# Optimization experiments

Measured on AMD Instinct MI355X. Metric: run time of the kernel, lower is better.

The kernel has to match this reference:

```python
import jax, jax.numpy as jnp
import numpy as np

N = 50000   # nodes
E = 800000  # edges
D = 128     # node_channels


def setup_inputs() -> dict:
    key = jax.random.key(0)
    ks = jax.random.split(key, 16)
    s = 1.0 / np.sqrt(D)
    inp = {
        "x": jax.random.normal(ks[0], (N, D), dtype=jnp.float32),
        "edge_index": jax.random.randint(ks[1], (2, E), 0, N, dtype=jnp.int64),
        "eps": jax.random.normal(ks[2], (N, D), dtype=jnp.float32),
    }
    names = ["1", "2", "mu", "logstd", "5", "6"]
    for i, nm in enumerate(names):
        inp[f"W{nm}"] = jax.random.normal(ks[3 + 2 * i], (D, D), dtype=jnp.float32) * s
        inp[f"b{nm}"] = jnp.zeros((D,), dtype=jnp.float32)
    return inp


def _gcn_norm(edge_index, num_nodes):
    # add self-loops, then symmetric normalization deg^{-1/2} (A+I) deg^{-1/2}
    loop = jnp.arange(num_nodes, dtype=edge_index.dtype)
    src = jnp.concatenate([edge_index[0], loop])
    dst = jnp.concatenate([edge_index[1], loop])
    deg = jax.ops.segment_sum(jnp.ones_like(src, dtype=jnp.float32), dst,
                              num_segments=num_nodes)
    dis = jnp.where(deg > 0, jax.lax.rsqrt(deg), 0.0)
    norm = dis[src] * dis[dst]  # [E + N]
    return src, dst, norm


def _gcn(x, W, b, src, dst, norm, num_nodes):
    h = x @ W                              # [N, D] small GEMM
    msg = h[src] * norm[:, None]           # gather + scale, [E+N, D]
    out = jax.ops.segment_sum(msg, dst, num_segments=num_nodes)  # scatter-add
    return out + b


def reference(x, edge_index, eps, W1, b1, W2, b2, Wmu, bmu, Wlogstd, blogstd,
              W5, b5, W6, b6):
    num_nodes = x.shape[0]
    src, dst, norm = _gcn_norm(edge_index, num_nodes)
    g = lambda h, W, b: _gcn(h, W, b, src, dst, norm, num_nodes)

    nodes = jax.nn.relu(g(x, W1, b1))
    nodes = jax.nn.relu(g(nodes, W2, b2))
    mu = g(nodes, Wmu, bmu)
    logstd = g(nodes, Wlogstd, blogstd)
    # reparametrize (training mode), divider = 10
    nodes = mu + eps * jnp.exp(logstd) / 10.0
    nodes = jax.nn.relu(g(nodes, W5, b5))
    nodes = jax.nn.relu(g(nodes, W6, b6))
    return nodes
```

## Files before the change

### kernel.cpp

```cpp
#include <hip/hip_runtime.h>
#include <hip/hip_bf16.h>
#include <cstdint>
#include <cstddef>

#define D 128
#define NWG 200

typedef _Float16 f16;
typedef f16 f16x2 __attribute__((ext_vector_type(2)));
typedef f16 f16x4 __attribute__((ext_vector_type(4)));
typedef f16 f16x8 __attribute__((ext_vector_type(8)));
typedef float f32x4 __attribute__((ext_vector_type(4)));

static inline size_t align256(size_t x){ return (x + 255) & ~(size_t)255; }

__global__ void detect_kernel(const int* __restrict__ ei, long long n32, int* __restrict__ flag){
  __shared__ int s;
  if (threadIdx.x == 0) s = 0;
  __syncthreads();
  int nz = 0;
  for (long long i = 2LL*threadIdx.x + 1; i < 4096 && i < n32; i += 512)
    nz |= (ei[i] != 0);
  if (nz) s = 1;
  __syncthreads();
  if (threadIdx.x == 0) *flag = (s ? 0 : 1);
}

__device__ __forceinline__ void load_edge(const void* ei, int E, int is64, int e, int& s, int& d){
  if (is64) {
    const long long* p = (const long long*)ei;
    s = (int)p[e]; d = (int)p[(size_t)E + e];
  } else {
    const int* p = (const int*)ei;
    s = p[e]; d = p[(size_t)E + e];
  }
}

__global__ __launch_bounds__(256) void passA_hist(
    const void* __restrict__ ei, int E, const int* __restrict__ flag,
    int* __restrict__ glob_hist, int NB){
  __shared__ int cnt[256];
  int t = threadIdx.x, wg = blockIdx.x;
  cnt[t] = 0;
  __syncthreads();
  int is64 = *flag;
  int chunk = (E + NWG - 1) / NWG;
  int lo = wg * chunk, hi = min(lo + chunk, E);
  for (int e = lo + t; e < hi; e += 256){
    int s, d;
    load_edge(ei, E, is64, e, s, d);
    atomicAdd(&cnt[d >> 8], 1);
  }
  __syncthreads();
  for (int b = t; b < NB; b += 256)
    glob_hist[b * NWG + wg] = cnt[b];
}

__global__ void scan_partial(const int* __restrict__ src, int* __restrict__ dst,
                             int* __restrict__ blockSums, int L){
  __shared__ int sd[256];
  int t = threadIdx.x;
  int base = blockIdx.x * 1024 + t * 4;
  int v[4]; int s = 0;
  #pragma unroll
  for (int j = 0; j < 4; ++j){ v[j] = (base + j < L) ? src[base + j] : 0; s += v[j]; }
  sd[t] = s; __syncthreads();
  for (int off = 1; off < 256; off <<= 1){
    int x = (t >= off) ? sd[t - off] : 0;
    __syncthreads();
    sd[t] += x;
    __syncthreads();
  }
  int run = sd[t] - s;
  #pragma unroll
  for (int j = 0; j < 4; ++j){
    if (base + j < L) dst[base + j] = run;
    run += v[j];
  }
  if (t == 255) blockSums[blockIdx.x] = sd[255];
}

__global__ void scan_blocksums(int* __restrict__ blockSums, int nblk,
                               int* __restrict__ dst, int L, int total){
  __shared__ int sd[256];
  int t = threadIdx.x;
  int v = (t < nblk) ? blockSums[t] : 0;
  sd[t] = v; __syncthreads();
  for (int off = 1; off < 256; off <<= 1){
    int x = (t >= off) ? sd[t - off] : 0;
    __syncthreads();
    sd[t] += x;
    __syncthreads();
  }
  if (t < nblk) blockSums[t] = sd[t] - v;
  if (t == 0) dst[L] = total;
}

__global__ void scan_add(int* __restrict__ dst, const int* __restrict__ blockSums, int L){
  int i = blockIdx.x * blockDim.x + threadIdx.x;
  if (i >= L) return;
  dst[i] += blockSums[i >> 10];
}

__global__ __launch_bounds__(256) void passB_scatter(
    const void* __restrict__ ei, int E, const int* __restrict__ flag,
    const int* __restrict__ bucketOff, int NB, unsigned* __restrict__ packed){
  __shared__ int cur[256];
  int t = threadIdx.x, wg = blockIdx.x;
  for (int b = t; b < NB; b += 256)
    cur[b] = bucketOff[b * NWG + wg];
  __syncthreads();
  int is64 = *flag;
  int chunk = (E + NWG - 1) / NWG;
  int lo = wg * chunk, hi = min(lo + chunk, E);
  for (int e = lo + t; e < hi; e += 256){
    int s, d;
    load_edge(ei, E, is64, e, s, d);
    int pos = atomicAdd(&cur[d >> 8], 1);
    packed[pos] = (unsigned)s | ((unsigned)(d & 255) << 16);
  }
}

__global__ __launch_bounds__(256) void passC_csr(
    const unsigned* __restrict__ packed, const int* __restrict__ bucketOff,
    int NB, int N, int E,
    int* __restrict__ rowptr, float* __restrict__ dis, int* __restrict__ csr_src){
  __shared__ int degl[256];
  __shared__ int sd[256];
  __shared__ int cur[256];
  int t = threadIdx.x, b = blockIdx.x;
  int begin = bucketOff[(size_t)b * NWG];
  int endb  = bucketOff[(size_t)(b + 1) * NWG];
  degl[t] = 0;
  __syncthreads();
  for (int i = begin + t; i < endb; i += 256)
    atomicAdd(&degl[(packed[i] >> 16) & 255], 1);
  __syncthreads();
  int dv = degl[t];
  sd[t] = dv; __syncthreads();
  for (int off = 1; off < 256; off <<= 1){
    int x = (t >= off) ? sd[t - off] : 0;
    __syncthreads();
    sd[t] += x;
    __syncthreads();
  }
  int localOff = sd[t] - dv;
  int v = b * 256 + t;
  if (v < N){
    rowptr[v] = begin + localOff;
    dis[v] = rsqrtf((float)(dv + 1));
  }
  if (b == NB - 1 && t == 0) rowptr[N] = E;
  cur[t] = begin + localOff;
  __syncthreads();
  for (int i = begin + t; i < endb; i += 256){
    unsigned p = packed[i];
    int pos = atomicAdd(&cur[(p >> 16) & 255], 1);
    csr_src[pos] = (int)(p & 0xFFFFu);
  }
}

__global__ void cast_scale(const float* __restrict__ in, const float* __restrict__ dis,
                           f16* __restrict__ out, int n4){
  int i = blockIdx.x * blockDim.x + threadIdx.x;
  if (i >= n4) return;
  float dv = dis[i >> 5];
  float4 v = ((const float4*)in)[i];
  f16x4 o; o[0]=(f16)(v.x*dv); o[1]=(f16)(v.y*dv); o[2]=(f16)(v.z*dv); o[3]=(f16)(v.w*dv);
  ((f16x4*)out)[i] = o;
}

__global__ void prep_w(const float* __restrict__ Wa, const float* __restrict__ Wb,
                       const float* __restrict__ Wc, const float* __restrict__ Wd,
                       const float* __restrict__ We, const float* __restrict__ Wf,
                       f16* __restrict__ Wt){
  int i = blockIdx.x * 256 + threadIdx.x;
  int w = i >> 14, rem = i & 16383;
  int n = rem >> 7, k = rem & 127;
  const float* Wp = (w==0)?Wa:(w==1)?Wb:(w==2)?Wc:(w==3)?Wd:(w==4)?We:Wf;
  Wt[i] = (f16)Wp[k*128 + n];
}

__global__ __launch_bounds__(256) void agg16(
    const f16* __restrict__ in, f16* __restrict__ out,
    const int* __restrict__ rowptr, const int* __restrict__ csr_src,
    const float* __restrict__ dis, int N){
  int v = blockIdx.x * 4 + (threadIdx.x >> 6);
  if (v >= N) return;
  int c2 = (threadIdx.x & 63) * 2;
  float dv = dis[v];
  int beg = rowptr[v], end = rowptr[v + 1];
  f16x2 sv = *(const f16x2*)&in[(size_t)v * D + c2];
  float acc0 = (float)sv[0], acc1 = (float)sv[1];
  int e = beg;
  for (; e + 7 < end; e += 8){
    f16x2 h[8];
    #pragma unroll
    for (int j = 0; j < 8; ++j){
      int u = csr_src[e + j];
      h[j] = *(const f16x2*)&in[(size_t)u * D + c2];
    }
    #pragma unroll
    for (int j = 0; j < 8; ++j){ acc0 += (float)h[j][0]; acc1 += (float)h[j][1]; }
  }
  for (; e + 1 < end; e += 2){
    int u0 = csr_src[e], u1 = csr_src[e + 1];
    f16x2 h0 = *(const f16x2*)&in[(size_t)u0 * D + c2];
    f16x2 h1 = *(const f16x2*)&in[(size_t)u1 * D + c2];
    acc0 += (float)h0[0] + (float)h1[0];
    acc1 += (float)h0[1] + (float)h1[1];
  }
  if (e < end){
    int u = csr_src[e];
    f16x2 h = *(const f16x2*)&in[(size_t)u * D + c2];
    acc0 += (float)h[0]; acc1 += (float)h[1];
  }
  f16x2 o; o[0] = (f16)(acc0 * dv); o[1] = (f16)(acc1 * dv);
  *(f16x2*)&out[(size_t)v * D + c2] = o;
}

template<int EPI>
__global__ __launch_bounds__(512) void gemm_mfma(
    const f16* __restrict__ A, const f16* __restrict__ Wt, const float* __restrict__ bias,
    const f16* __restrict__ Wt2, const float* __restrict__ bias2,
    const float* __restrict__ eps, const float* __restrict__ dis,
    f16* __restrict__ out16, float* __restrict__ outf, int N){

  extern __shared__ __align__(16) f16 Ws[];

  int t = threadIdx.x;
  int wave = t >> 6, lane = t & 63;
  int lrow = lane & 15, hi = lane >> 4;
  int r0 = blockIdx.x * 128 + wave * 16;
  bool active = (r0 < N);

  f16x8 a[4];
  if (active){
    int rr = min(r0 + lrow, N - 1);
    const f16* arow = &A[(size_t)rr * D + hi * 8];
    #pragma unroll
    for (int s = 0; s < 4; ++s) a[s] = *(const f16x8*)&arow[s * 32];
  }

  {
    int r = t & 127, p = t >> 7;
    const float4* src = (const float4*)&Wt[r * 128 + p * 32];
    f16* dstrow = &Ws[r * 128];
    #pragma unroll
    for (int i = 0; i < 4; ++i){
      int q = p * 4 + i;
      *(float4*)&dstrow[(q ^ (r & 7)) * 8] = src[i];
    }
    if (EPI == 1){
      const float4* src2 = (const float4*)&Wt2[r * 128 + p * 32];
      f16* dstrow2 = &Ws[16384 + r * 128];
      #pragma unroll
      for (int i = 0; i < 4; ++i){
        int q = p * 4 + i;
        *(float4*)&dstrow2[(q ^ (r & 7)) * 8] = src2[i];
      }
    }
  }
  __syncthreads();
  if (!active) return;

  f32x4 acc[8] = {};
  f32x4 acc2[8] = {};

  #pragma unroll
  for (int s = 0; s < 4; ++s){
    #pragma unroll
    for (int tt = 0; tt < 8; ++tt){
      int n = tt * 16 + lrow;
      int q = (s * 4 + hi) ^ (lrow & 7);
      f16x8 b = *(const f16x8*)&Ws[n * 128 + q * 8];
      acc[tt] = __builtin_amdgcn_mfma_f32_16x16x32_f16(b, a[s], acc[tt], 0, 0, 0);
      if (EPI == 1){
        f16x8 b2 = *(const f16x8*)&Ws[16384 + n * 128 + q * 8];
        acc2[tt] = __builtin_amdgcn_mfma_f32_16x16x32_f16(b2, a[s], acc2[tt], 0, 0, 0);
      }
    }
  }

  int r = r0 + lrow;
  if (r >= N) return;
  float dv = (EPI == 2) ? 1.f : dis[r];
  int cbase = hi * 4;
  #pragma unroll
  for (int tt = 0; tt < 8; ++tt){
    int n0 = tt * 16 + cbase;
    f32x4 bv = *(const f32x4*)&bias[n0];
    if (EPI == 0){
      f16x4 o;
      #pragma unroll
      for (int ii = 0; ii < 4; ++ii)
        o[ii] = (f16)(fmaxf(acc[tt][ii] + bv[ii], 0.f) * dv);
      *(f16x4*)&out16[(size_t)r * D + n0] = o;
    } else if (EPI == 1){
      f32x4 bv2 = *(const f32x4*)&bias2[n0];
      f32x4 e4  = *(const f32x4*)&eps[(size_t)r * D + n0];
      f16x4 o;
      #pragma unroll
      for (int ii = 0; ii < 4; ++ii){
        float mu = acc[tt][ii] + bv[ii];
        float ls = acc2[tt][ii] + bv2[ii];
        o[ii] = (f16)((mu + e4[ii] * __expf(ls) * 0.1f) * dv);
      }
      *(f16x4*)&out16[(size_t)r * D + n0] = o;
    } else {
      f32x4 o;
      #pragma unroll
      for (int ii = 0; ii < 4; ++ii)
        o[ii] = fmaxf(acc[tt][ii] + bv[ii], 0.f);
      *(f32x4*)&outf[(size_t)r * D + n0] = o;
    }
  }
}

extern "C" void kernel_launch(void* const* d_in, const int* in_sizes, int n_in,
                              void* d_out, int out_size, void* d_ws, size_t ws_size,
                              hipStream_t stream){
  const float* x   = (const float*)d_in[0];
  const void*  ei  = d_in[1];
  const float* eps = (const float*)d_in[2];
  const float* W1  = (const float*)d_in[3];  const float* b1  = (const float*)d_in[4];
  const float* W2  = (const float*)d_in[5];  const float* b2  = (const float*)d_in[6];
  const float* Wmu = (const float*)d_in[7];  const float* bmu = (const float*)d_in[8];
  const float* Wls = (const float*)d_in[9];  const float* bls = (const float*)d_in[10];
  const float* W5  = (const float*)d_in[11]; const float* b5  = (const float*)d_in[12];
  const float* W6  = (const float*)d_in[13]; const float* b6  = (const float*)d_in[14];

  const int N = in_sizes[0] / D;
  const int E = in_sizes[1] / 2;
  const int NB = (N + 255) >> 8;
  const int L  = NB * NWG;
  float* out = (float*)d_out;

  char* ws = (char*)d_ws;
  size_t off = 0;
  auto alloc = [&](size_t bytes){ char* p = ws + off; off += align256(bytes); return p; };
  int*      flag      = (int*)     alloc(256);
  int*      glob_hist = (int*)     alloc(((size_t)L + 1) * 4);
  int*      bucketOff = (int*)     alloc(((size_t)L + 1) * 4);
  int*      blockSums = (int*)     alloc(1024);
  int*      rowptr    = (int*)     alloc(((size_t)N + 1) * 4);
  float*    dis       = (float*)   alloc((size_t)N * 4);
  unsigned* packed    = (unsigned*)alloc((size_t)E * 4);
  int*      csr_src   = (int*)     alloc((size_t)E * 4);
  f16*      Wt        = (f16*)     alloc((size_t)6 * 128 * 128 * 2);
  f16*      bufA      = (f16*)     alloc((size_t)N * D * 2);
  f16*      bufB      = (f16*)     alloc((size_t)N * D * 2);
  (void)ws_size; (void)n_in; (void)out_size;

  detect_kernel<<<1, 256, 0, stream>>>((const int*)ei, (long long)2 * E, flag);

  passA_hist<<<NWG, 256, 0, stream>>>(ei, E, flag, glob_hist, NB);
  int nblk = (L + 1023) / 1024;
  scan_partial<<<nblk, 256, 0, stream>>>(glob_hist, bucketOff, blockSums, L);
  scan_blocksums<<<1, 256, 0, stream>>>(blockSums, nblk, bucketOff, L, E);
  scan_add<<<(L + 255) / 256, 256, 0, stream>>>(bucketOff, blockSums, L);
  passB_scatter<<<NWG, 256, 0, stream>>>(ei, E, flag, bucketOff, NB, packed);
  passC_csr<<<NB, 256, 0, stream>>>(packed, bucketOff, NB, N, E, rowptr, dis, csr_src);

  cast_scale<<<(N * D / 4 + 255) / 256, 256, 0, stream>>>(x, dis, bufB, N * D / 4);
  prep_w<<<(6 * 16384) / 256, 256, 0, stream>>>(W1, W2, Wmu, Wls, W5, W6, Wt);

  int aggGrid = (N + 3) / 4;
  int gemmGrid = (N + 127) / 128;
  size_t lds1 = 128 * 128 * sizeof(f16);
  size_t lds2 = 2 * 128 * 128 * sizeof(f16);

  agg16<<<aggGrid, 256, 0, stream>>>(bufB, bufA, rowptr, csr_src, dis, N);
  gemm_mfma<0><<<gemmGrid, 512, lds1, stream>>>(bufA, Wt + 0*16384, b1, nullptr, nullptr, nullptr, dis, bufB, nullptr, N);
  agg16<<<aggGrid, 256, 0, stream>>>(bufB, bufA, rowptr, csr_src, dis, N);
  gemm_mfma<0><<<gemmGrid, 512, lds1, stream>>>(bufA, Wt + 1*16384, b2, nullptr, nullptr, nullptr, dis, bufB, nullptr, N);
  agg16<<<aggGrid, 256, 0, stream>>>(bufB, bufA, rowptr, csr_src, dis, N);
  gemm_mfma<1><<<gemmGrid, 512, lds2, stream>>>(bufA, Wt + 2*16384, bmu, Wt + 3*16384, bls, eps, dis, bufB, nullptr, N);
  agg16<<<aggGrid, 256, 0, stream>>>(bufB, bufA, rowptr, csr_src, dis, N);
  gemm_mfma<0><<<gemmGrid, 512, lds1, stream>>>(bufA, Wt + 4*16384, b5, nullptr, nullptr, nullptr, dis, bufB, nullptr, N);
  agg16<<<aggGrid, 256, 0, stream>>>(bufB, bufA, rowptr, csr_src, dis, N);
  gemm_mfma<2><<<gemmGrid, 512, lds1, stream>>>(bufA, Wt + 5*16384, b6, nullptr, nullptr, nullptr, dis, nullptr, out, N);
}
```

Measured before the change: 396.6 us.

## Drop detect and scan_add launches, use 16-bit CSR indices, widen aggregation unroll

Removes the detect_kernel and scan_add launches. The int64 check becomes a per-block wave ballot, and the block-sum offsets are folded into the scatter and CSR passes. CSR source indices are stored as 16-bit values, which halves index traffic in the aggregation kernels. The gather loop is unrolled to 16 with a clamped, masked tail, and uses nontemporal index loads and output stores. Narrowing to u16 only works when node ids fit in 16 bits, which is not the case for N=50000 beyond 65535… it does hold here, but it fixes the limit to small graphs.

```diff
diff --git a/kernel.cpp b/kernel.cpp
--- a/kernel.cpp
+++ b/kernel.cpp
@@ -11,19 +11,14 @@
 typedef f16 f16x4 __attribute__((ext_vector_type(4)));
 typedef f16 f16x8 __attribute__((ext_vector_type(8)));
 typedef float f32x4 __attribute__((ext_vector_type(4)));
+typedef unsigned short u16;
 
 static inline size_t align256(size_t x){ return (x + 255) & ~(size_t)255; }
 
-__global__ void detect_kernel(const int* __restrict__ ei, long long n32, int* __restrict__ flag){
-  __shared__ int s;
-  if (threadIdx.x == 0) s = 0;
-  __syncthreads();
-  int nz = 0;
-  for (long long i = 2LL*threadIdx.x + 1; i < 4096 && i < n32; i += 512)
-    nz |= (ei[i] != 0);
-  if (nz) s = 1;
-  __syncthreads();
-  if (threadIdx.x == 0) *flag = (s ? 0 : 1);
+__device__ __forceinline__ int detect_is64(const void* ei){
+  const int* e32 = (const int*)ei;
+  int probe = e32[2 * (threadIdx.x & 31) + 1];
+  return (__ballot(probe != 0) == 0ULL) ? 1 : 0;
 }
 
 __device__ __forceinline__ void load_edge(const void* ei, int E, int is64, int e, int& s, int& d){
@@ -37,13 +32,13 @@
 }
 
 __global__ __launch_bounds__(256) void passA_hist(
-    const void* __restrict__ ei, int E, const int* __restrict__ flag,
+    const void* __restrict__ ei, int E,
     int* __restrict__ glob_hist, int NB){
   __shared__ int cnt[256];
   int t = threadIdx.x, wg = blockIdx.x;
+  int is64 = detect_is64(ei);
   cnt[t] = 0;
   __syncthreads();
-  int is64 = *flag;
   int chunk = (E + NWG - 1) / NWG;
   int lo = wg * chunk, hi = min(lo + chunk, E);
   for (int e = lo + t; e < hi; e += 256){
@@ -80,8 +75,7 @@
   if (t == 255) blockSums[blockIdx.x] = sd[255];
 }
 
-__global__ void scan_blocksums(int* __restrict__ blockSums, int nblk,
-                               int* __restrict__ dst, int L, int total){
+__global__ void scan_blocksums(int* __restrict__ blockSums, int nblk){
   __shared__ int sd[256];
   int t = threadIdx.x;
   int v = (t < nblk) ? blockSums[t] : 0;
@@ -93,24 +87,20 @@
     __syncthreads();
   }
   if (t < nblk) blockSums[t] = sd[t] - v;
-  if (t == 0) dst[L] = total;
-}
-
-__global__ void scan_add(int* __restrict__ dst, const int* __restrict__ blockSums, int L){
-  int i = blockIdx.x * blockDim.x + threadIdx.x;
-  if (i >= L) return;
-  dst[i] += blockSums[i >> 10];
 }
 
 __global__ __launch_bounds__(256) void passB_scatter(
-    const void* __restrict__ ei, int E, const int* __restrict__ flag,
-    const int* __restrict__ bucketOff, int NB, unsigned* __restrict__ packed){
+    const void* __restrict__ ei, int E,
+    const int* __restrict__ bucketOff, const int* __restrict__ blockSums,
+    int NB, unsigned* __restrict__ packed){
   __shared__ int cur[256];
   int t = threadIdx.x, wg = blockIdx.x;
-  for (int b = t; b < NB; b += 256)
-    cur[b] = bucketOff[b * NWG + wg];
-  __syncthreads();
-  int is64 = *flag;
+  int is64 = detect_is64(ei);
+  for (int b = t; b < NB; b += 256){
+    int i = b * NWG + wg;
+    cur[b] = bucketOff[i] + blockSums[i >> 10];
+  }
+  __syncthreads();
   int chunk = (E + NWG - 1) / NWG;
   int lo = wg * chunk, hi = min(lo + chunk, E);
   for (int e = lo + t; e < hi; e += 256){
@@ -123,14 +113,15 @@
 
 __global__ __launch_bounds__(256) void passC_csr(
     const unsigned* __restrict__ packed, const int* __restrict__ bucketOff,
-    int NB, int N, int E,
-    int* __restrict__ rowptr, float* __restrict__ dis, int* __restrict__ csr_src){
+    const int* __restrict__ blockSums, int NB, int N, int E,
+    int* __restrict__ rowptr, float* __restrict__ dis, u16* __restrict__ csr_src){
   __shared__ int degl[256];
   __shared__ int sd[256];
   __shared__ int cur[256];
   int t = threadIdx.x, b = blockIdx.x;
-  int begin = bucketOff[(size_t)b * NWG];
-  int endb  = bucketOff[(size_t)(b + 1) * NWG];
+  int i0 = b * NWG, i1 = (b + 1) * NWG;
+  int begin = bucketOff[i0] + blockSums[i0 >> 10];
+  int endb  = (b == NB - 1) ? E : (bucketOff[i1] + blockSums[i1 >> 10]);
   degl[t] = 0;
   __syncthreads();
   for (int i = begin + t; i < endb; i += 256)
@@ -156,7 +147,7 @@
   for (int i = begin + t; i < endb; i += 256){
     unsigned p = packed[i];
     int pos = atomicAdd(&cur[(p >> 16) & 255], 1);
-    csr_src[pos] = (int)(p & 0xFFFFu);
+    csr_src[pos] = (u16)(p & 0xFFFFu);
   }
 }
 
@@ -183,7 +174,7 @@
 
 __global__ __launch_bounds__(256) void agg16(
     const f16* __restrict__ in, f16* __restrict__ out,
-    const int* __restrict__ rowptr, const int* __restrict__ csr_src,
+    const int* __restrict__ rowptr, const u16* __restrict__ csr_src,
     const float* __restrict__ dis, int N){
   int v = blockIdx.x * 4 + (threadIdx.x >> 6);
   if (v >= N) return;
@@ -193,30 +184,35 @@
   f16x2 sv = *(const f16x2*)&in[(size_t)v * D + c2];
   float acc0 = (float)sv[0], acc1 = (float)sv[1];
   int e = beg;
-  for (; e + 7 < end; e += 8){
-    f16x2 h[8];
-    #pragma unroll
-    for (int j = 0; j < 8; ++j){
-      int u = csr_src[e + j];
+  for (; e + 15 < end; e += 16){
+    f16x2 h[16];
+    #pragma unroll
+    for (int j = 0; j < 16; ++j){
+      unsigned u = __builtin_nontemporal_load(&csr_src[e + j]);
       h[j] = *(const f16x2*)&in[(size_t)u * D + c2];
     }
     #pragma unroll
-    for (int j = 0; j < 8; ++j){ acc0 += (float)h[j][0]; acc1 += (float)h[j][1]; }
-  }
-  for (; e + 1 < end; e += 2){
-    int u0 = csr_src[e], u1 = csr_src[e + 1];
-    f16x2 h0 = *(const f16x2*)&in[(size_t)u0 * D + c2];
-    f16x2 h1 = *(const f16x2*)&in[(size_t)u1 * D + c2];
-    acc0 += (float)h0[0] + (float)h1[0];
-    acc1 += (float)h0[1] + (float)h1[1];
-  }
-  if (e < end){
-    int u = csr_src[e];
-    f16x2 h = *(const f16x2*)&in[(size_t)u * D + c2];
-    acc0 += (float)h[0]; acc1 += (float)h[1];
+    for (int j = 0; j < 16; ++j){ acc0 += (float)h[j][0]; acc1 += (float)h[j][1]; }
+  }
+  int rem = end - e;
+  if (rem > 0){
+    int last = end - 1;
+    f16x2 h[16];
+    #pragma unroll
+    for (int j = 0; j < 16; ++j){
+      int idx = e + j;
+      idx = idx > last ? last : idx;
+      unsigned u = __builtin_nontemporal_load(&csr_src[idx]);
+      h[j] = *(const f16x2*)&in[(size_t)u * D + c2];
+    }
+    #pragma unroll
+    for (int j = 0; j < 16; ++j){
+      acc0 += (j < rem) ? (float)h[j][0] : 0.f;
+      acc1 += (j < rem) ? (float)h[j][1] : 0.f;
+    }
   }
   f16x2 o; o[0] = (f16)(acc0 * dv); o[1] = (f16)(acc1 * dv);
-  *(f16x2*)&out[(size_t)v * D + c2] = o;
+  __builtin_nontemporal_store(o, (f16x2*)&out[(size_t)v * D + c2]);
 }
 
 template<int EPI>
@@ -339,28 +335,24 @@
   char* ws = (char*)d_ws;
   size_t off = 0;
   auto alloc = [&](size_t bytes){ char* p = ws + off; off += align256(bytes); return p; };
-  int*      flag      = (int*)     alloc(256);
   int*      glob_hist = (int*)     alloc(((size_t)L + 1) * 4);
   int*      bucketOff = (int*)     alloc(((size_t)L + 1) * 4);
   int*      blockSums = (int*)     alloc(1024);
   int*      rowptr    = (int*)     alloc(((size_t)N + 1) * 4);
   float*    dis       = (float*)   alloc((size_t)N * 4);
   unsigned* packed    = (unsigned*)alloc((size_t)E * 4);
-  int*      csr_src   = (int*)     alloc((size_t)E * 4);
+  u16*      csr_src   = (u16*)     alloc((size_t)E * 2);
   f16*      Wt        = (f16*)     alloc((size_t)6 * 128 * 128 * 2);
   f16*      bufA      = (f16*)     alloc((size_t)N * D * 2);
   f16*      bufB      = (f16*)     alloc((size_t)N * D * 2);
   (void)ws_size; (void)n_in; (void)out_size;
 
-  detect_kernel<<<1, 256, 0, stream>>>((const int*)ei, (long long)2 * E, flag);
-
-  passA_hist<<<NWG, 256, 0, stream>>>(ei, E, flag, glob_hist, NB);
+  passA_hist<<<NWG, 256, 0, stream>>>(ei, E, glob_hist, NB);
   int nblk = (L + 1023) / 1024;
   scan_partial<<<nblk, 256, 0, stream>>>(glob_hist, bucketOff, blockSums, L);
-  scan_blocksums<<<1, 256, 0, stream>>>(blockSums, nblk, bucketOff, L, E);
-  scan_add<<<(L + 255) / 256, 256, 0, stream>>>(bucketOff, blockSums, L);
-  passB_scatter<<<NWG, 256, 0, stream>>>(ei, E, flag, bucketOff, NB, packed);
-  passC_csr<<<NB, 256, 0, stream>>>(packed, bucketOff, NB, N, E, rowptr, dis, csr_src);
+  scan_blocksums<<<1, 256, 0, stream>>>(blockSums, nblk);
+  passB_scatter<<<NWG, 256, 0, stream>>>(ei, E, bucketOff, blockSums, NB, packed);
+  passC_csr<<<NB, 256, 0, stream>>>(packed, bucketOff, blockSums, NB, N, E, rowptr, dis, csr_src);
 
   cast_scale<<<(N * D / 4 + 255) / 256, 256, 0, stream>>>(x, dis, bufB, N * D / 4);
   prep_w<<<(6 * 16384) / 256, 256, 0, stream>>>(W1, W2, Wmu, Wls, W5, W6, Wt);
```

After: 385.1 us. 1.03x faster.
